# Optimization experiments

Hardware: AMD Instinct MI355X
Metric: run time of the kernel (lower is better)

Reference implementation:

```python
import jax, jax.numpy as jnp
import numpy as np

HEADS = 16
DIM_HEAD = 64
SCALE = DIM_HEAD ** -0.5
NEG = -jnp.finfo(jnp.float32).max


def setup_inputs() -> dict:
    key = jax.random.key(0)
    ks = jax.random.split(key, 5)
    b, n, dim = 2, 2048, 1024
    inner = HEADS * DIM_HEAD
    s = dim ** -0.5  # keep pre-softmax logits well-scaled
    return {
        "x": jax.random.normal(ks[0], (b, n, dim), jnp.float32),
        "mask": jnp.ones((b, n), dtype=bool),
        "Wq": jax.random.normal(ks[1], (dim, inner), jnp.float32) * s,
        "Wk": jax.random.normal(ks[2], (dim, inner), jnp.float32) * s,
        "Wv": jax.random.normal(ks[3], (dim, inner), jnp.float32) * s,
        "Wo": jax.random.normal(ks[4], (inner, dim), jnp.float32) * s,
    }


def reference(x, mask, Wq, Wk, Wv, Wo):
    b, n, _ = x.shape
    # projections, split heads: b n (h d) -> b h n d
    def split(t):
        return t.reshape(b, n, HEADS, DIM_HEAD).transpose(0, 2, 1, 3)
    q = split(x @ Wq)
    k = split(x @ Wk)
    v = split(x @ Wv)
    dots = jnp.einsum("bhid,bhjd->bhij", q, k) * SCALE  # [b,h,n,n]
    # padding mask: b j -> b 1 1 j
    dots = jnp.where(mask[:, None, None, :], dots, NEG)
    # causal mask (strict upper triangle masked)
    causal = jnp.triu(jnp.ones((n, n), dtype=bool), k=1)
    dots = jnp.where(causal, NEG, dots)
    attn = jax.nn.softmax(dots, axis=-1)
    out = jnp.einsum("bhij,bhjd->bhid", attn, v)
    out = out.transpose(0, 2, 1, 3).reshape(b, n, HEADS * DIM_HEAD)
    return out @ Wo
```

## Files before the change

### kernel.cpp

```cpp
#include <hip/hip_runtime.h>
#include <hip/hip_bf16.h>

typedef __bf16 bf16x8 __attribute__((ext_vector_type(8)));
typedef float f32x4 __attribute__((ext_vector_type(4)));
typedef unsigned short u16;
typedef unsigned int u32;

#define MFMA16(A, B, C) __builtin_amdgcn_mfma_f32_16x16x32_bf16((A), (B), (C), 0, 0, 0)

#define BATCH 2
#define SEQ   2048
#define DIM   1024
#define NHEAD 16
#define DHEAD 64
#define MROWS 4096
#define Q_SCALE 0.18033688f

__device__ __forceinline__ u16 f2bf(float f) {
    unsigned int u = __float_as_uint(f);
    u += 0x7fff + ((u >> 16) & 1);
    return (u16)(u >> 16);
}

__device__ __forceinline__ u32 pk2bf(float a, float b) {
    __hip_bfloat162 c = __float22bfloat162_rn(float2{a, b});
    u32 r;
    __builtin_memcpy(&r, &c, 4);
    return r;
}

__device__ __forceinline__ void glds16(const u16* g, u16* l) {
    __builtin_amdgcn_global_load_lds(
        (const __attribute__((address_space(1))) u32*)g,
        (__attribute__((address_space(3))) u32*)l, 16, 0, 0);
}

__global__ __launch_bounds__(256) void cvt_x(const float* __restrict__ x,
                                             u16* __restrict__ xb) {
    int i = (blockIdx.x * 256 + threadIdx.x) * 8;
    float4 a = *(const float4*)(x + i);
    float4 b = *(const float4*)(x + i + 4);
    u16 o[8] = {f2bf(a.x), f2bf(a.y), f2bf(a.z), f2bf(a.w),
                f2bf(b.x), f2bf(b.y), f2bf(b.z), f2bf(b.w)};
    *(uint4*)(xb + i) = *(uint4*)o;
}

__global__ __launch_bounds__(256) void cvt_w_t(const float* __restrict__ wq,
                                               const float* __restrict__ wk,
                                               const float* __restrict__ wv,
                                               const float* __restrict__ wo,
                                               u16* __restrict__ wt) {
    __shared__ u16 tile[64][65];
    const float* W = (blockIdx.z == 0) ? wq : (blockIdx.z == 1) ? wk
                   : (blockIdx.z == 2) ? wv : wo;
    u16* out = wt + (size_t)blockIdx.z * DIM * DIM;
    int k0 = blockIdx.x * 64;
    int n0 = blockIdx.y * 64;
    int t = threadIdx.x;
    int c = t & 63, r4 = t >> 6;
#pragma unroll
    for (int i = 0; i < 16; i++) {
        int row = i * 4 + r4;
        tile[row][c] = f2bf(W[(size_t)(k0 + row) * DIM + n0 + c]);
    }
    __syncthreads();
#pragma unroll
    for (int i = 0; i < 16; i++) {
        int row = i * 4 + r4;
        out[(size_t)(n0 + row) * DIM + k0 + c] = tile[c][row];
    }
}

__global__ __launch_bounds__(256) void gemm_qkv(const u16* __restrict__ xb,
                                                const u16* __restrict__ wt,
                                                u16* __restrict__ qb,
                                                u16* __restrict__ kb,
                                                u16* __restrict__ vtb) {
    __shared__ __align__(16) u16 As[128 * 32];
    __shared__ __align__(16) u16 Bs[128 * 32];
    const int z = blockIdx.z;
    const u16* W = wt + (size_t)z * DIM * DIM;
    const int m0 = blockIdx.y * 128, n0 = blockIdx.x * 128;
    const int t = threadIdx.x, w = t >> 6, lane = t & 63;
    const int quad = lane >> 4, l16 = lane & 15;
    const int wm = (w >> 1) * 64, wn = (w & 1) * 64;
    const int srow = lane >> 2, skc = (lane & 3) * 8;

    f32x4 acc[4][4] = {};
    for (int k0 = 0; k0 < DIM; k0 += 32) {
        if (k0) __syncthreads();
#pragma unroll
        for (int j = 0; j < 2; j++) {
            int rb = w * 32 + j * 16;
            glds16(&xb[(size_t)(m0 + rb + srow) * DIM + k0 + skc], &As[rb * 32]);
            glds16(&W[(size_t)(n0 + rb + srow) * DIM + k0 + skc], &Bs[rb * 32]);
        }
        __syncthreads();

        bf16x8 af[4], bfr[4];
#pragma unroll
        for (int mt = 0; mt < 4; mt++)
            af[mt] = *(const bf16x8*)&As[(wm + mt * 16 + l16) * 32 + quad * 8];
#pragma unroll
        for (int nt = 0; nt < 4; nt++)
            bfr[nt] = *(const bf16x8*)&Bs[(wn + nt * 16 + l16) * 32 + quad * 8];
#pragma unroll
        for (int mt = 0; mt < 4; mt++)
#pragma unroll
            for (int nt = 0; nt < 4; nt++)
                acc[mt][nt] = MFMA16(af[mt], bfr[nt], acc[mt][nt]);
    }
    const float sc = (z == 0) ? Q_SCALE : 1.0f;
#pragma unroll
    for (int mt = 0; mt < 4; mt++)
#pragma unroll
        for (int nt = 0; nt < 4; nt++)
#pragma unroll
            for (int r = 0; r < 4; r++) {
                int gm = m0 + wm + mt * 16 + quad * 4 + r;
                int gc = n0 + wn + nt * 16 + l16;
                int bi = gm >> 11, si = gm & (SEQ - 1);
                int h = gc >> 6, d = gc & 63;
                u16 v = f2bf(acc[mt][nt][r] * sc);
                if (z == 0)
                    qb[(((size_t)bi * NHEAD + h) * SEQ + si) * DHEAD + d] = v;
                else if (z == 1)
                    kb[(((size_t)bi * NHEAD + h) * SEQ + si) * DHEAD + d] = v;
                else
                    vtb[(((size_t)bi * NHEAD + h) * DHEAD + d) * SEQ + si] = v;
            }
}

#define LPAD 72
#define OSTR 68
__global__ __launch_bounds__(256) void attn(const u16* __restrict__ qg,
                                            const u16* __restrict__ kg,
                                            const u16* __restrict__ vtg,
                                            u16* __restrict__ og) {
    __shared__ __align__(16) u16 Ks[2][64 * LPAD];
    __shared__ __align__(16) u16 Vs[2][64 * LPAD];
    __shared__ __align__(16) u16 Ps[64 * LPAD];
    __shared__ __align__(16) float Os[64 * OSTR];
    __shared__ float Ls[64];

    const int bh = blockIdx.y;
    const int t = threadIdx.x, w = t >> 6, lane = t & 63;
    const int quad = lane >> 4, l16 = lane & 15;
    const int wq32 = (w >> 1) * 32, kh = w & 1, kh32 = kh * 32;
    const int srow = t >> 2, sc16 = (t & 3) * 16;
    const size_t qkbase = (size_t)bh * SEQ;
    const size_t vbase = (size_t)bh * DHEAD;
    const int bi = bh >> 4, hh = bh & 15;

    uint4 pk0, pk1, pv0, pv1;
    auto prefetch = [&](int j0) {
        const u16* kp = &kg[(qkbase + j0 + srow) * DHEAD + sc16];
        pk0 = *(const uint4*)kp;
        pk1 = *(const uint4*)(kp + 8);
        const u16* vp = &vtg[(vbase + srow) * SEQ + j0 + sc16];
        pv0 = *(const uint4*)vp;
        pv1 = *(const uint4*)(vp + 8);
    };

    for (int half = 0; half < 2; half++) {
        const int qt = half ? (31 - (int)blockIdx.x) : (int)blockIdx.x;
        const int q0 = qt * 64;
        const int last = qt;
        const int rowmin = q0 + wq32;

        bf16x8 bq[2][2];
#pragma unroll
        for (int ct = 0; ct < 2; ct++) {
            const u16* qp = qg + (qkbase + q0 + wq32 + ct * 16 + l16) * DHEAD;
            bq[ct][0] = *(const bf16x8*)(qp + quad * 8);
            bq[ct][1] = *(const bf16x8*)(qp + 32 + quad * 8);
        }

        f32x4 accO[4][2] = {};
        float l_part[2] = {0.f, 0.f};

        prefetch(0);
        __syncthreads();

        for (int jt = 0; jt <= last; jt++) {
            const int buf = jt & 1;
            u16* ksb = &Ks[buf][0];
            u16* vsb = &Vs[buf][0];
            *(uint4*)&ksb[srow * LPAD + sc16] = pk0;
            *(uint4*)&ksb[srow * LPAD + sc16 + 8] = pk1;
            *(uint4*)&vsb[srow * LPAD + sc16] = pv0;
            *(uint4*)&vsb[srow * LPAD + sc16 + 8] = pv1;
            __syncthreads();
            if (jt < last) prefetch((jt + 1) * 64);

            const int j0 = jt * 64;
            if (j0 + kh32 > rowmin + 31) continue;
            const bool need_mask = (j0 + kh32 + 31 > rowmin);

            bf16x8 ak[2][2];
#pragma unroll
            for (int nt = 0; nt < 2; nt++) {
                const u16* kr = &ksb[(kh32 + nt * 16 + l16) * LPAD];
                ak[nt][0] = *(const bf16x8*)(kr + quad * 8);
                ak[nt][1] = *(const bf16x8*)(kr + 32 + quad * 8);
            }
            f32x4 s[2][2];
#pragma unroll
            for (int nt = 0; nt < 2; nt++)
#pragma unroll
                for (int ct = 0; ct < 2; ct++) {
                    f32x4 a = {};
                    a = MFMA16(ak[nt][0], bq[ct][0], a);
                    a = MFMA16(ak[nt][1], bq[ct][1], a);
                    s[nt][ct] = a;
                }

            if (need_mask) {
#pragma unroll
                for (int ct = 0; ct < 2; ct++) {
                    int qv = q0 + wq32 + ct * 16 + l16;
#pragma unroll
                    for (int nt = 0; nt < 2; nt++) {
                        int kb = j0 + kh32 + nt * 16 + quad * 4;
                        float p[4];
#pragma unroll
                        for (int r = 0; r < 4; r++)
                            p[r] = (kb + r > qv) ? 0.f
                                 : __builtin_amdgcn_exp2f(s[nt][ct][r]);
                        l_part[ct] += (p[0] + p[1]) + (p[2] + p[3]);
                        uint2 pkd = {pk2bf(p[0], p[1]), pk2bf(p[2], p[3])};
                        *(uint2*)&Ps[(wq32 + ct * 16 + l16) * LPAD + kh32 +
                                     nt * 16 + quad * 4] = pkd;
                    }
                }
            } else {
#pragma unroll
                for (int ct = 0; ct < 2; ct++)
#pragma unroll
                    for (int nt = 0; nt < 2; nt++) {
                        float p[4];
#pragma unroll
                        for (int r = 0; r < 4; r++)
                            p[r] = __builtin_amdgcn_exp2f(s[nt][ct][r]);
                        l_part[ct] += (p[0] + p[1]) + (p[2] + p[3]);
                        uint2 pkd = {pk2bf(p[0], p[1]), pk2bf(p[2], p[3])};
                        *(uint2*)&Ps[(wq32 + ct * 16 + l16) * LPAD + kh32 +
                                     nt * 16 + quad * 4] = pkd;
                    }
            }

            bf16x8 bp[2];
#pragma unroll
            for (int ct = 0; ct < 2; ct++)
                bp[ct] = *(const bf16x8*)&Ps[(wq32 + ct * 16 + l16) * LPAD +
                                             kh32 + quad * 8];
#pragma unroll
            for (int mt = 0; mt < 4; mt++) {
                bf16x8 av = *(const bf16x8*)&vsb[(mt * 16 + l16) * LPAD +
                                                 kh32 + quad * 8];
#pragma unroll
                for (int ct = 0; ct < 2; ct++)
                    accO[mt][ct] = MFMA16(av, bp[ct], accO[mt][ct]);
            }
        }

        float l2[2];
#pragma unroll
        for (int ct = 0; ct < 2; ct++) {
            float l = l_part[ct];
            l += __shfl_xor(l, 16);
            l += __shfl_xor(l, 32);
            l2[ct] = l;
        }
        if (kh == 1) {
            if (quad == 0) {
                Ls[wq32 + l16] = l2[0];
                Ls[wq32 + 16 + l16] = l2[1];
            }
#pragma unroll
            for (int mt = 0; mt < 4; mt++)
#pragma unroll
                for (int ct = 0; ct < 2; ct++)
                    *(float4*)&Os[(wq32 + ct * 16 + l16) * OSTR + mt * 16 +
                                  quad * 4] =
                        float4{accO[mt][ct][0], accO[mt][ct][1],
                               accO[mt][ct][2], accO[mt][ct][3]};
        }
        __syncthreads();
        if (kh == 0) {
#pragma unroll
            for (int ct = 0; ct < 2; ct++) {
                int q = q0 + wq32 + ct * 16 + l16;
                float rl = 1.0f / (l2[ct] + Ls[wq32 + ct * 16 + l16]);
                size_t obase = ((size_t)bi * SEQ + q) * DIM + hh * DHEAD;
#pragma unroll
                for (int mt = 0; mt < 4; mt++) {
                    float4 o = *(float4*)&Os[(wq32 + ct * 16 + l16) * OSTR +
                                             mt * 16 + quad * 4];
                    float v0 = (accO[mt][ct][0] + o.x) * rl;
                    float v1 = (accO[mt][ct][1] + o.y) * rl;
                    float v2 = (accO[mt][ct][2] + o.z) * rl;
                    float v3 = (accO[mt][ct][3] + o.w) * rl;
                    uint2 pkd = {pk2bf(v0, v1), pk2bf(v2, v3)};
                    *(uint2*)&og[obase + mt * 16 + quad * 4] = pkd;
                }
            }
        }
    }
}

__global__ __launch_bounds__(256) void gemm_out(const u16* __restrict__ ob,
                                                const u16* __restrict__ wot,
                                                float* __restrict__ out) {
    __shared__ __align__(16) u16 As[64 * 32];
    __shared__ __align__(16) u16 Bs[128 * 32];
    const int m0 = blockIdx.y * 64, n0 = blockIdx.x * 128;
    const int t = threadIdx.x, w = t >> 6, lane = t & 63;
    const int quad = lane >> 4, l16 = lane & 15;
    const int wm = (w >> 1) * 32, wn = (w & 1) * 64;
    const int srow = lane >> 2, skc = (lane & 3) * 8;

    f32x4 acc[2][4] = {};
    for (int k0 = 0; k0 < DIM; k0 += 32) {
        if (k0) __syncthreads();
        glds16(&ob[(size_t)(m0 + w * 16 + srow) * DIM + k0 + skc], &As[w * 16 * 32]);
#pragma unroll
        for (int j = 0; j < 2; j++) {
            int rb = w * 32 + j * 16;
            glds16(&wot[(size_t)(n0 + rb + srow) * DIM + k0 + skc], &Bs[rb * 32]);
        }
        __syncthreads();

        bf16x8 af[2], bfr[4];
#pragma unroll
        for (int mt = 0; mt < 2; mt++)
            af[mt] = *(const bf16x8*)&As[(wm + mt * 16 + l16) * 32 + quad * 8];
#pragma unroll
        for (int nt = 0; nt < 4; nt++)
            bfr[nt] = *(const bf16x8*)&Bs[(wn + nt * 16 + l16) * 32 + quad * 8];
#pragma unroll
        for (int mt = 0; mt < 2; mt++)
#pragma unroll
            for (int nt = 0; nt < 4; nt++)
                acc[mt][nt] = MFMA16(af[mt], bfr[nt], acc[mt][nt]);
    }
#pragma unroll
    for (int mt = 0; mt < 2; mt++)
#pragma unroll
        for (int nt = 0; nt < 4; nt++)
#pragma unroll
            for (int r = 0; r < 4; r++) {
                int gm = m0 + wm + mt * 16 + quad * 4 + r;
                int gc = n0 + wn + nt * 16 + l16;
                out[(size_t)gm * DIM + gc] = acc[mt][nt][r];
            }
}

extern "C" void kernel_launch(void* const* d_in, const int* in_sizes, int n_in,
                              void* d_out, int out_size, void* d_ws, size_t ws_size,
                              hipStream_t stream) {
    const float* x  = (const float*)d_in[0];
    const float* wq = (const float*)d_in[2];
    const float* wk = (const float*)d_in[3];
    const float* wv = (const float*)d_in[4];
    const float* wo = (const float*)d_in[5];
    float* out = (float*)d_out;

    char* ws = (char*)d_ws;
    u16* xb  = (u16*)(ws);
    u16* wt  = (u16*)(ws + (8ull  << 20));
    u16* qb  = (u16*)(ws + (16ull << 20));
    u16* kb  = (u16*)(ws + (24ull << 20));
    u16* vtb = (u16*)(ws + (32ull << 20));
    u16* obf = (u16*)(ws + (40ull << 20));

    cvt_x<<<MROWS * DIM / (256 * 8), 256, 0, stream>>>(x, xb);
    cvt_w_t<<<dim3(16, 16, 4), 256, 0, stream>>>(wq, wk, wv, wo, wt);
    gemm_qkv<<<dim3(DIM / 128, MROWS / 128, 3), 256, 0, stream>>>(xb, wt, qb, kb, vtb);
    attn<<<dim3(16, BATCH * NHEAD), 256, 0, stream>>>(qb, kb, vtb, obf);
    gemm_out<<<dim3(DIM / 128, MROWS / 64), 256, 0, stream>>>(
        obf, wt + 3ull * DIM * DIM, out);
}
```

Before: 187.1 us.

## Unpair attention query tiles, remap grid, and alias output scratch onto P buffer

The attention kernel no longer has each block process a balanced pair of query tiles. It now launches one block per (head, query tile) with a custom linear-to-(bh, qt) mapping that interleaves heads. The fp32 output-combine scratch and the row-sum array are aliased onto the P staging area, with OSTR reduced to 66, and an extra barrier guards that reuse. The goal is lower LDS per block so more blocks fit per CU, plus finer-grained scheduling, at the cost of losing the explicit causal load pairing and possibly misaligned 16-byte LDS stores.

```diff
diff --git a/kernel.cpp b/kernel.cpp
--- a/kernel.cpp
+++ b/kernel.cpp
@@ -132,18 +132,21 @@
 }
 
 #define LPAD 72
-#define OSTR 68
+#define OSTR 66
 __global__ __launch_bounds__(256) void attn(const u16* __restrict__ qg,
                                             const u16* __restrict__ kg,
                                             const u16* __restrict__ vtg,
                                             u16* __restrict__ og) {
-    __shared__ __align__(16) u16 Ks[2][64 * LPAD];
-    __shared__ __align__(16) u16 Vs[2][64 * LPAD];
-    __shared__ __align__(16) u16 Ps[64 * LPAD];
-    __shared__ __align__(16) float Os[64 * OSTR];
-    __shared__ float Ls[64];
-
-    const int bh = blockIdx.y;
+    __shared__ __align__(16) u16 lds[4 * 64 * LPAD + 8448 + 128];
+    u16* Ks0 = &lds[0];
+    u16* Vs0 = &lds[2 * 64 * LPAD];
+    u16* Ps  = &lds[4 * 64 * LPAD];
+    float* Osp = (float*)&lds[4 * 64 * LPAD];
+    float* Lsp = (float*)&lds[4 * 64 * LPAD + 8448];
+
+    const int linear = blockIdx.x + 32 * blockIdx.y;
+    const int bh = (linear & 7) * 4 + (linear >> 8);
+    const int qt = (linear >> 3) & 31;
     const int t = threadIdx.x, w = t >> 6, lane = t & 63;
     const int quad = lane >> 4, l16 = lane & 15;
     const int wq32 = (w >> 1) * 32, kh = w & 1, kh32 = kh * 32;
@@ -162,148 +165,145 @@
         pv1 = *(const uint4*)(vp + 8);
     };
 
-    for (int half = 0; half < 2; half++) {
-        const int qt = half ? (31 - (int)blockIdx.x) : (int)blockIdx.x;
-        const int q0 = qt * 64;
-        const int last = qt;
-        const int rowmin = q0 + wq32;
-
-        bf16x8 bq[2][2];
+    const int q0 = qt * 64;
+    const int last = qt;
+    const int rowmin = q0 + wq32;
+
+    bf16x8 bq[2][2];
+#pragma unroll
+    for (int ct = 0; ct < 2; ct++) {
+        const u16* qp = qg + (qkbase + q0 + wq32 + ct * 16 + l16) * DHEAD;
+        bq[ct][0] = *(const bf16x8*)(qp + quad * 8);
+        bq[ct][1] = *(const bf16x8*)(qp + 32 + quad * 8);
+    }
+
+    f32x4 accO[4][2] = {};
+    float l_part[2] = {0.f, 0.f};
+
+    prefetch(0);
+
+    for (int jt = 0; jt <= last; jt++) {
+        const int buf = jt & 1;
+        u16* ksb = &Ks0[buf * 64 * LPAD];
+        u16* vsb = &Vs0[buf * 64 * LPAD];
+        *(uint4*)&ksb[srow * LPAD + sc16] = pk0;
+        *(uint4*)&ksb[srow * LPAD + sc16 + 8] = pk1;
+        *(uint4*)&vsb[srow * LPAD + sc16] = pv0;
+        *(uint4*)&vsb[srow * LPAD + sc16 + 8] = pv1;
+        __syncthreads();
+        if (jt < last) prefetch((jt + 1) * 64);
+
+        const int j0 = jt * 64;
+        if (j0 + kh32 > rowmin + 31) continue;
+        const bool need_mask = (j0 + kh32 + 31 > rowmin);
+
+        bf16x8 ak[2][2];
+#pragma unroll
+        for (int nt = 0; nt < 2; nt++) {
+            const u16* kr = &ksb[(kh32 + nt * 16 + l16) * LPAD];
+            ak[nt][0] = *(const bf16x8*)(kr + quad * 8);
+            ak[nt][1] = *(const bf16x8*)(kr + 32 + quad * 8);
+        }
+        f32x4 s[2][2];
+#pragma unroll
+        for (int nt = 0; nt < 2; nt++)
+#pragma unroll
+            for (int ct = 0; ct < 2; ct++) {
+                f32x4 a = {};
+                a = MFMA16(ak[nt][0], bq[ct][0], a);
+                a = MFMA16(ak[nt][1], bq[ct][1], a);
+                s[nt][ct] = a;
+            }
+
+        if (need_mask) {
+#pragma unroll
+            for (int ct = 0; ct < 2; ct++) {
+                int qv = q0 + wq32 + ct * 16 + l16;
+#pragma unroll
+                for (int nt = 0; nt < 2; nt++) {
+                    int kb = j0 + kh32 + nt * 16 + quad * 4;
+                    float p[4];
+#pragma unroll
+                    for (int r = 0; r < 4; r++)
+                        p[r] = (kb + r > qv) ? 0.f
+                             : __builtin_amdgcn_exp2f(s[nt][ct][r]);
+                    l_part[ct] += (p[0] + p[1]) + (p[2] + p[3]);
+                    uint2 pkd = {pk2bf(p[0], p[1]), pk2bf(p[2], p[3])};
+                    *(uint2*)&Ps[(wq32 + ct * 16 + l16) * LPAD + kh32 +
+                                 nt * 16 + quad * 4] = pkd;
+                }
+            }
+        } else {
+#pragma unroll
+            for (int ct = 0; ct < 2; ct++)
+#pragma unroll
+                for (int nt = 0; nt < 2; nt++) {
+                    float p[4];
+#pragma unroll
+                    for (int r = 0; r < 4; r++)
+                        p[r] = __builtin_amdgcn_exp2f(s[nt][ct][r]);
+                    l_part[ct] += (p[0] + p[1]) + (p[2] + p[3]);
+                    uint2 pkd = {pk2bf(p[0], p[1]), pk2bf(p[2], p[3])};
+                    *(uint2*)&Ps[(wq32 + ct * 16 + l16) * LPAD + kh32 +
+                                 nt * 16 + quad * 4] = pkd;
+                }
+        }
+
+        bf16x8 bp[2];
+#pragma unroll
+        for (int ct = 0; ct < 2; ct++)
+            bp[ct] = *(const bf16x8*)&Ps[(wq32 + ct * 16 + l16) * LPAD +
+                                         kh32 + quad * 8];
+#pragma unroll
+        for (int mt = 0; mt < 4; mt++) {
+            bf16x8 av = *(const bf16x8*)&vsb[(mt * 16 + l16) * LPAD +
+                                             kh32 + quad * 8];
+#pragma unroll
+            for (int ct = 0; ct < 2; ct++)
+                accO[mt][ct] = MFMA16(av, bp[ct], accO[mt][ct]);
+        }
+    }
+
+    float l2[2];
+#pragma unroll
+    for (int ct = 0; ct < 2; ct++) {
+        float l = l_part[ct];
+        l += __shfl_xor(l, 16);
+        l += __shfl_xor(l, 32);
+        l2[ct] = l;
+    }
+    __syncthreads();
+    if (kh == 1) {
+        if (quad == 0) {
+            Lsp[wq32 + l16] = l2[0];
+            Lsp[wq32 + 16 + l16] = l2[1];
+        }
+#pragma unroll
+        for (int mt = 0; mt < 4; mt++)
+#pragma unroll
+            for (int ct = 0; ct < 2; ct++)
+                *(float4*)&Osp[(wq32 + ct * 16 + l16) * OSTR + mt * 16 +
+                               quad * 4] =
+                    float4{accO[mt][ct][0], accO[mt][ct][1],
+                           accO[mt][ct][2], accO[mt][ct][3]};
+    }
+    __syncthreads();
+    if (kh == 0) {
 #pragma unroll
         for (int ct = 0; ct < 2; ct++) {
-            const u16* qp = qg + (qkbase + q0 + wq32 + ct * 16 + l16) * DHEAD;
-            bq[ct][0] = *(const bf16x8*)(qp + quad * 8);
-            bq[ct][1] = *(const bf16x8*)(qp + 32 + quad * 8);
-        }
-
-        f32x4 accO[4][2] = {};
-        float l_part[2] = {0.f, 0.f};
-
-        prefetch(0);
-        __syncthreads();
-
-        for (int jt = 0; jt <= last; jt++) {
-            const int buf = jt & 1;
-            u16* ksb = &Ks[buf][0];
-            u16* vsb = &Vs[buf][0];
-            *(uint4*)&ksb[srow * LPAD + sc16] = pk0;
-            *(uint4*)&ksb[srow * LPAD + sc16 + 8] = pk1;
-            *(uint4*)&vsb[srow * LPAD + sc16] = pv0;
-            *(uint4*)&vsb[srow * LPAD + sc16 + 8] = pv1;
-            __syncthreads();
-            if (jt < last) prefetch((jt + 1) * 64);
-
-            const int j0 = jt * 64;
-            if (j0 + kh32 > rowmin + 31) continue;
-            const bool need_mask = (j0 + kh32 + 31 > rowmin);
-
-            bf16x8 ak[2][2];
-#pragma unroll
-            for (int nt = 0; nt < 2; nt++) {
-                const u16* kr = &ksb[(kh32 + nt * 16 + l16) * LPAD];
-                ak[nt][0] = *(const bf16x8*)(kr + quad * 8);
-                ak[nt][1] = *(const bf16x8*)(kr + 32 + quad * 8);
-            }
-            f32x4 s[2][2];
-#pragma unroll
-            for (int nt = 0; nt < 2; nt++)
-#pragma unroll
-                for (int ct = 0; ct < 2; ct++) {
-                    f32x4 a = {};
-                    a = MFMA16(ak[nt][0], bq[ct][0], a);
-                    a = MFMA16(ak[nt][1], bq[ct][1], a);
-                    s[nt][ct] = a;
-                }
-
-            if (need_mask) {
-#pragma unroll
-                for (int ct = 0; ct < 2; ct++) {
-                    int qv = q0 + wq32 + ct * 16 + l16;
-#pragma unroll
-                    for (int nt = 0; nt < 2; nt++) {
-                        int kb = j0 + kh32 + nt * 16 + quad * 4;
-                        float p[4];
-#pragma unroll
-                        for (int r = 0; r < 4; r++)
-                            p[r] = (kb + r > qv) ? 0.f
-                                 : __builtin_amdgcn_exp2f(s[nt][ct][r]);
-                        l_part[ct] += (p[0] + p[1]) + (p[2] + p[3]);
-                        uint2 pkd = {pk2bf(p[0], p[1]), pk2bf(p[2], p[3])};
-                        *(uint2*)&Ps[(wq32 + ct * 16 + l16) * LPAD + kh32 +
-                                     nt * 16 + quad * 4] = pkd;
-                    }
-                }
-            } else {
-#pragma unroll
-                for (int ct = 0; ct < 2; ct++)
-#pragma unroll
-                    for (int nt = 0; nt < 2; nt++) {
-                        float p[4];
-#pragma unroll
-                        for (int r = 0; r < 4; r++)
-                            p[r] = __builtin_amdgcn_exp2f(s[nt][ct][r]);
-                        l_part[ct] += (p[0] + p[1]) + (p[2] + p[3]);
-                        uint2 pkd = {pk2bf(p[0], p[1]), pk2bf(p[2], p[3])};
-                        *(uint2*)&Ps[(wq32 + ct * 16 + l16) * LPAD + kh32 +
-                                     nt * 16 + quad * 4] = pkd;
-                    }
-            }
-
-            bf16x8 bp[2];
-#pragma unroll
-            for (int ct = 0; ct < 2; ct++)
-                bp[ct] = *(const bf16x8*)&Ps[(wq32 + ct * 16 + l16) * LPAD +
-                                             kh32 + quad * 8];
+            int q = q0 + wq32 + ct * 16 + l16;
+            float rl = 1.0f / (l2[ct] + Lsp[wq32 + ct * 16 + l16]);
+            size_t obase = ((size_t)bi * SEQ + q) * DIM + hh * DHEAD;
 #pragma unroll
             for (int mt = 0; mt < 4; mt++) {
-                bf16x8 av = *(const bf16x8*)&vsb[(mt * 16 + l16) * LPAD +
-                                                 kh32 + quad * 8];
-#pragma unroll
-                for (int ct = 0; ct < 2; ct++)
-                    accO[mt][ct] = MFMA16(av, bp[ct], accO[mt][ct]);
-            }
-        }
-
-        float l2[2];
-#pragma unroll
-        for (int ct = 0; ct < 2; ct++) {
-            float l = l_part[ct];
-            l += __shfl_xor(l, 16);
-            l += __shfl_xor(l, 32);
-            l2[ct] = l;
-        }
-        if (kh == 1) {
-            if (quad == 0) {
-                Ls[wq32 + l16] = l2[0];
-                Ls[wq32 + 16 + l16] = l2[1];
-            }
-#pragma unroll
-            for (int mt = 0; mt < 4; mt++)
-#pragma unroll
-                for (int ct = 0; ct < 2; ct++)
-                    *(float4*)&Os[(wq32 + ct * 16 + l16) * OSTR + mt * 16 +
-                                  quad * 4] =
-                        float4{accO[mt][ct][0], accO[mt][ct][1],
-                               accO[mt][ct][2], accO[mt][ct][3]};
-        }
-        __syncthreads();
-        if (kh == 0) {
-#pragma unroll
-            for (int ct = 0; ct < 2; ct++) {
-                int q = q0 + wq32 + ct * 16 + l16;
-                float rl = 1.0f / (l2[ct] + Ls[wq32 + ct * 16 + l16]);
-                size_t obase = ((size_t)bi * SEQ + q) * DIM + hh * DHEAD;
-#pragma unroll
-                for (int mt = 0; mt < 4; mt++) {
-                    float4 o = *(float4*)&Os[(wq32 + ct * 16 + l16) * OSTR +
-                                             mt * 16 + quad * 4];
-                    float v0 = (accO[mt][ct][0] + o.x) * rl;
-                    float v1 = (accO[mt][ct][1] + o.y) * rl;
-                    float v2 = (accO[mt][ct][2] + o.z) * rl;
-                    float v3 = (accO[mt][ct][3] + o.w) * rl;
-                    uint2 pkd = {pk2bf(v0, v1), pk2bf(v2, v3)};
-                    *(uint2*)&og[obase + mt * 16 + quad * 4] = pkd;
-                }
+                float4 o = *(float4*)&Osp[(wq32 + ct * 16 + l16) * OSTR +
+                                          mt * 16 + quad * 4];
+                float v0 = (accO[mt][ct][0] + o.x) * rl;
+                float v1 = (accO[mt][ct][1] + o.y) * rl;
+                float v2 = (accO[mt][ct][2] + o.z) * rl;
+                float v3 = (accO[mt][ct][3] + o.w) * rl;
+                uint2 pkd = {pk2bf(v0, v1), pk2bf(v2, v3)};
+                *(uint2*)&og[obase + mt * 16 + quad * 4] = pkd;
             }
         }
     }
@@ -377,7 +377,7 @@
     cvt_x<<<MROWS * DIM / (256 * 8), 256, 0, stream>>>(x, xb);
     cvt_w_t<<<dim3(16, 16, 4), 256, 0, stream>>>(wq, wk, wv, wo, wt);
     gemm_qkv<<<dim3(DIM / 128, MROWS / 128, 3), 256, 0, stream>>>(xb, wt, qb, kb, vtb);
-    attn<<<dim3(16, BATCH * NHEAD), 256, 0, stream>>>(qb, kb, vtb, obf);
+    attn<<<dim3(32, 32), 256, 0, stream>>>(qb, kb, vtb, obf);
     gemm_out<<<dim3(DIM / 128, MROWS / 64), 256, 0, stream>>>(
         obf, wt + 3ull * DIM * DIM, out);
 }
```

Result: slower. 193.8 us (+3.6%).
